# Kernel tuning notes

Measured on AMD Instinct MI355X. Metric: run time of the kernel, lower is better.

## Reference

```python
import jax, jax.numpy as jnp
import numpy as np

NUM_AUDIOS = 64
NODES_PER = 800
N = NUM_AUDIOS * NODES_PER  # 51200
DEG = 8
E = N * DEG  # 409600
IN_C, HID, OUT, HEADS = 512, 256, 256, 2
NEG_SLOPE = 0.2  # PyG GATConv default


def setup_inputs() -> dict:
    key = jax.random.key(0)
    ks = jax.random.split(key, 12)
    x = jax.random.normal(ks[0], (N, IN_C), jnp.float32)
    # edges strictly inside each audio's node block (PyG batching: no cross-graph edges)
    src_l = jax.random.randint(ks[1], (NUM_AUDIOS, NODES_PER * DEG), 0, NODES_PER)
    dst_l = jax.random.randint(ks[2], (NUM_AUDIOS, NODES_PER * DEG), 0, NODES_PER)
    off = (jnp.arange(NUM_AUDIOS) * NODES_PER)[:, None]
    edge_index = jnp.stack([(src_l + off).reshape(-1), (dst_l + off).reshape(-1)]).astype(jnp.int32)
    batch = jnp.repeat(jnp.arange(NUM_AUDIOS), NODES_PER).astype(jnp.int32)

    def gl(k, shape, fan):
        return (jax.random.normal(k, shape, jnp.float32) / np.sqrt(fan)).astype(jnp.float32)

    W1 = gl(ks[3], (IN_C, HEADS * HID), IN_C)
    a_s1 = gl(ks[4], (HEADS, HID), HID)
    a_d1 = gl(ks[5], (HEADS, HID), HID)
    b1 = jnp.zeros((HID,), jnp.float32)
    W2 = gl(ks[6], (HID, HEADS * OUT), HID)
    a_s2 = gl(ks[7], (HEADS, OUT), OUT)
    a_d2 = gl(ks[8], (HEADS, OUT), OUT)
    b2 = jnp.zeros((OUT,), jnp.float32)
    w_att = gl(ks[9], (OUT, 1), OUT)
    b_att = jnp.zeros((1,), jnp.float32)
    w_cls = gl(ks[10], (OUT, 2), OUT)
    b_cls = jnp.zeros((2,), jnp.float32)
    return dict(x=x, edge_index=edge_index, batch=batch,
                W1=W1, a_s1=a_s1, a_d1=a_d1, b1=b1,
                W2=W2, a_s2=a_s2, a_d2=a_d2, b2=b2,
                w_att=w_att, b_att=b_att, w_cls=w_cls, b_cls=b_cls)


def _gat(x, src, dst, W, a_s, a_d, b):
    """PyG GATConv(heads=H, concat=False): linear -> per-edge LeakyReLU scores ->
    softmax over incoming edges (with self-loops) -> scatter-sum -> head-mean + bias."""
    n = x.shape[0]
    H, C = a_s.shape
    h = (x @ W).reshape(n, H, C)                      # [N,H,C]
    al_s = jnp.einsum('nhc,hc->nh', h, a_s)           # [N,H]
    al_d = jnp.einsum('nhc,hc->nh', h, a_d)
    loop = jnp.arange(n, dtype=src.dtype)             # add self-loops (default)
    s = jnp.concatenate([src, loop])
    d = jnp.concatenate([dst, loop])
    e = jax.nn.leaky_relu(al_s[s] + al_d[d], NEG_SLOPE)  # [E+N,H]
    mx = jax.ops.segment_max(e, d, num_segments=n)
    w = jnp.exp(e - mx[d])
    den = jax.ops.segment_sum(w, d, num_segments=n)
    alpha = w / den[d]
    out = jax.ops.segment_sum(h[s] * alpha[:, :, None], d, num_segments=n)  # [N,H,C]
    return out.mean(axis=1) + b


def reference(x, edge_index, batch, W1, a_s1, a_d1, b1, W2, a_s2, a_d2, b2,
              w_att, b_att, w_cls, b_cls):
    src, dst = edge_index[0], edge_index[1]
    h = jax.nn.relu(_gat(x, src, dst, W1, a_s1, a_d1, b1))
    node_emb = _gat(h, src, dst, W2, a_s2, a_d2, b2)
    # per-audio temporal attention: softmax over nodes within each audio segment.
    # (edges never cross audio boundaries, so the per-subgraph GAT re-run in the
    #  original Python loop equals the full-graph GAT restricted to each segment.)
    logits = node_emb @ w_att + b_att                 # [N,1]
    mx = jax.ops.segment_max(logits, batch, num_segments=NUM_AUDIOS)
    w = jnp.exp(logits - mx[batch])
    den = jax.ops.segment_sum(w, batch, num_segments=NUM_AUDIOS)
    attn = w / den[batch]                             # [N,1]
    attended = jax.ops.segment_sum(attn * node_emb, batch, num_segments=NUM_AUDIOS)  # [A,OUT]
    audio_result = attended @ w_cls + b_cls           # [A,2]
    return node_emb, audio_result
```

## Files before the change

### kernel.cpp

```cpp
#include <hip/hip_runtime.h>
#include <cstdint>
#include <cstddef>

#define NUM_AUDIOS 64
#define NODES_PER  800
#define NN         51200
#define EE         409600

typedef __attribute__((ext_vector_type(8))) unsigned short ushort8;
typedef __attribute__((ext_vector_type(8))) __bf16 bf16x8;
typedef __attribute__((ext_vector_type(4))) float f32x4;

__device__ __forceinline__ float b2f(unsigned short h) {
  return __uint_as_float(((unsigned)h) << 16);
}
__device__ __forceinline__ unsigned short f2b(float f) {
  unsigned u = __float_as_uint(f);
  u += 0x7fffu + ((u >> 16) & 1u);
  return (unsigned short)(u >> 16);
}
__device__ __forceinline__ float lrelu(float v) { return v > 0.f ? v : 0.2f * v; }

#define P_AS1 0
#define P_AD1 512
#define P_B1  1024
#define P_AS2 1536
#define P_AD2 2048
#define P_B2  2560
#define P_WATT 3072
#define P_BATT 3328
#define P_WCLS 3336
#define P_BCLS 3848

#define ZERO_F4 132096
#define ZERO_BLOCKS 516

__global__ __launch_bounds__(256) void prolog0_k(float4* __restrict__ zbase,
                                                 const unsigned short* __restrict__ x,
                                                 int* __restrict__ flag) {
  const int i = blockIdx.x * 256 + threadIdx.x;
  if (i < ZERO_F4) zbase[i] = (float4){0.f, 0.f, 0.f, 0.f};
  if (blockIdx.x == 0) {
    __shared__ int s;
    if (threadIdx.x == 0) s = 0;
    __syncthreads();
    int big = 0;
    for (int k = threadIdx.x; k < 4096; k += 256) {
      const float v = b2f(x[k]);
      if (!(__builtin_fabsf(v) <= 1e4f)) big = 1;
    }
    if (big) atomicOr(&s, 1);
    __syncthreads();
    if (threadIdx.x == 0) *flag = s;
  }
}

#define PB_PAR  10
#define PB_T1   (PB_PAR + 1024)
#define PB_T2   (PB_T1 + 512)
#define PB_HIST (PB_T2 + 1600)

__global__ __launch_bounds__(256) void prep_k(
    const void* __restrict__ W1, unsigned short* __restrict__ W1T,
    const void* __restrict__ W2, unsigned short* __restrict__ W2T,
    const void* p0, const void* p1, const void* p2, const void* p3, const void* p4,
    const void* p5, const void* p6, const void* p7, const void* p8, const void* p9,
    unsigned short* __restrict__ params,
    const int* __restrict__ dst, int* __restrict__ counts,
    const int* __restrict__ flagp) {
  const int b = blockIdx.x, tid = threadIdx.x;
  const int f = *flagp;
  if (b < PB_PAR) {
    const void* srcs[10] = {p0, p1, p2, p3, p4, p5, p6, p7, p8, p9};
    const int offs[10] = {P_AS1, P_AD1, P_B1, P_AS2, P_AD2, P_B2, P_WATT, P_BATT, P_WCLS, P_BCLS};
    const int lens[10] = {512, 512, 256, 512, 512, 256, 256, 1, 512, 2};
    const int s = b;
    for (int i = tid; i < lens[s]; i += 256)
      params[offs[s] + i] = f ? f2b(((const float*)srcs[s])[i])
                              : ((const unsigned short*)srcs[s])[i];
  } else if (b < PB_T1) {
    const int idx = (b - PB_PAR) * 256 + tid;
    const int n = idx >> 9, k = idx & 511;
    W1T[idx] = f ? f2b(((const float*)W1)[(size_t)k * 512 + n])
                 : ((const unsigned short*)W1)[(size_t)k * 512 + n];
  } else if (b < PB_T2) {
    const int idx = (b - PB_T1) * 256 + tid;
    const int n = idx >> 8, k = idx & 255;
    W2T[idx] = f ? f2b(((const float*)W2)[(size_t)k * 512 + n])
                 : ((const unsigned short*)W2)[(size_t)k * 512 + n];
  } else {
    const int e = (b - PB_T2) * 256 + tid;
    atomicAdd(&counts[dst[e]], 1);
  }
}

__global__ __launch_bounds__(256) void rowptr_k(const int* __restrict__ counts, int* __restrict__ row_ptr) {
  __shared__ int sh[800];
  __shared__ int pre[200];
  const int a = blockIdx.x, t = threadIdx.x;
  for (int i = t; i < 800; i += 256) sh[i] = counts[a * 800 + i];
  __syncthreads();
  if (t < 200) pre[t] = sh[t * 4] + sh[t * 4 + 1] + sh[t * 4 + 2] + sh[t * 4 + 3];
  __syncthreads();
  if (t == 0) {
    int run = 0;
    for (int i = 0; i < 200; ++i) { const int v = pre[i]; pre[i] = run; run += v; }
  }
  __syncthreads();
  if (t < 200) {
    int b = a * 6400 + pre[t];
#pragma unroll
    for (int j = 0; j < 4; ++j) { row_ptr[a * 800 + t * 4 + j] = b; b += sh[t * 4 + j]; }
  }
}

__global__ __launch_bounds__(256) void scatter_k(const int* __restrict__ src, const int* __restrict__ dst,
                                                 const int* __restrict__ row_ptr, int* __restrict__ cursor,
                                                 int* __restrict__ ssrc) {
  const int e = blockIdx.x * 256 + threadIdx.x;
  const int d = dst[e];
  const int p = atomicAdd(&cursor[d], 1);
  ssrc[row_ptr[d] + p] = src[e];
}

__device__ __forceinline__ void mfma_tile256(const unsigned short* As, const unsigned short* Bs,
                                             int wm, int wn, int row, int quad, f32x4 acc[8][4]) {
  bf16x8 af[8], bq[4];
  const int pa = (quad ^ (row & 3)) * 8;
#pragma unroll
  for (int i = 0; i < 8; ++i)
    af[i] = *(const bf16x8*)&As[(wm * 128 + i * 16 + row) * 32 + pa];
#pragma unroll
  for (int j = 0; j < 4; ++j)
    bq[j] = *(const bf16x8*)&Bs[(wn * 64 + j * 16 + row) * 32 + pa];
#pragma unroll
  for (int i = 0; i < 8; ++i)
#pragma unroll
    for (int j = 0; j < 4; ++j)
      acc[i][j] = __builtin_amdgcn_mfma_f32_16x16x32_bf16(af[i], bq[j], acc[i][j], 0, 0, 0);
}

__global__ __launch_bounds__(512, 2) void gemm_bt(const void* __restrict__ Araw,
                                                  const unsigned short* __restrict__ BT,
                                                  unsigned short* __restrict__ C,
                                                  int K, int Nn,
                                                  const unsigned short* __restrict__ a_s,
                                                  const unsigned short* __restrict__ a_d,
                                                  float* __restrict__ al_s,
                                                  float* __restrict__ al_d,
                                                  const int* __restrict__ aflag) {
  __shared__ unsigned short smem[32768];
  const int tid = threadIdx.x;
  const int wave = tid >> 6, lane = tid & 63;
  const int bid = blockIdx.x;
  const int g = bid & 7, bt = bid >> 3;
  const int mt = bt >> 1, nt = bt & 1;
  const int m0 = (g * 25 + mt) * 256;
  const int n0 = nt * 256;
  const int wm = wave >> 2, wn = wave & 3;
  const int row = lane & 15, quad = lane >> 4;
  const int col = lane & 15;
  f32x4 acc[8][4];
#pragma unroll
  for (int i = 0; i < 8; ++i)
#pragma unroll
    for (int j = 0; j < 4; ++j) acc[i][j] = (f32x4){0.f, 0.f, 0.f, 0.f};

  const bool a_is_f32 = (aflag != nullptr) && (*aflag != 0);
  const unsigned short* A16 = (const unsigned short*)Araw;
  const float* A32 = (const float*)Araw;
  const int srow0 = tid >> 2;
  const int kph = tid & 3;

  if (!a_is_f32) {
    const int nk = K >> 5;
    auto stage = [&](int buf, int k0) {
      unsigned short* Asb = smem + buf * 16384;
      unsigned short* Bsb = Asb + 8192;
#pragma unroll
      for (int p = 0; p < 2; ++p) {
        const int arow = p * 128 + srow0;
        const int kc = ((kph ^ (arow & 3)) * 8);
        __builtin_amdgcn_global_load_lds(
            (const __attribute__((address_space(1))) void*)(A16 + (size_t)(m0 + arow) * K + k0 + kc),
            (__attribute__((address_space(3))) void*)(Asb + (p * 512 + tid) * 8),
            16, 0, 0);
        __builtin_amdgcn_global_load_lds(
            (const __attribute__((address_space(1))) void*)(BT + (size_t)(n0 + arow) * K + k0 + kc),
            (__attribute__((address_space(3))) void*)(Bsb + (p * 512 + tid) * 8),
            16, 0, 0);
      }
    };
    stage(0, 0);
    for (int t = 0; t < nk; ++t) {
      const int cur = t & 1;
      if (t + 1 < nk) {
        stage(cur ^ 1, (t + 1) << 5);
        asm volatile("s_waitcnt vmcnt(4)" ::: "memory");
      } else {
        asm volatile("s_waitcnt vmcnt(0)" ::: "memory");
      }
      __builtin_amdgcn_sched_barrier(0);
      __builtin_amdgcn_s_barrier();
      __builtin_amdgcn_sched_barrier(0);
      mfma_tile256(smem + cur * 16384, smem + cur * 16384 + 8192, wm, wn, row, quad, acc);
      __builtin_amdgcn_sched_barrier(0);
      __builtin_amdgcn_s_barrier();
    }
  } else {
    unsigned short* As = smem;
    unsigned short* Bs = smem + 8192;
    for (int k0 = 0; k0 < K; k0 += 32) {
      ushort8 pk[2];
#pragma unroll
      for (int p = 0; p < 2; ++p) {
        const int arow = p * 128 + srow0;
        const int kc = ((kph ^ (arow & 3)) * 8);
        const float* ap = A32 + (size_t)(m0 + arow) * K + k0 + kc;
        const float4 f0 = *(const float4*)ap;
        const float4 f1 = *(const float4*)(ap + 4);
        pk[p][0] = f2b(f0.x); pk[p][1] = f2b(f0.y); pk[p][2] = f2b(f0.z); pk[p][3] = f2b(f0.w);
        pk[p][4] = f2b(f1.x); pk[p][5] = f2b(f1.y); pk[p][6] = f2b(f1.z); pk[p][7] = f2b(f1.w);
      }
      __syncthreads();
#pragma unroll
      for (int p = 0; p < 2; ++p) {
        const int arow = p * 128 + srow0;
        const int kc = ((kph ^ (arow & 3)) * 8);
        __builtin_amdgcn_global_load_lds(
            (const __attribute__((address_space(1))) void*)(BT + (size_t)(n0 + arow) * K + k0 + kc),
            (__attribute__((address_space(3))) void*)(Bs + (size_t)(p * 512 + tid) * 8),
            16, 0, 0);
        *(ushort8*)&As[(size_t)(p * 512 + tid) * 8] = pk[p];
      }
      __syncthreads();
      mfma_tile256(As, Bs, wm, wn, row, quad, acc);
    }
  }

  __syncthreads();

  {
    float* alb = (float*)smem;
    float as4[4], ad4[4];
#pragma unroll
    for (int j = 0; j < 4; ++j) {
      const int gn = n0 + wn * 64 + j * 16 + col;
      as4[j] = b2f(a_s[gn]);
      ad4[j] = b2f(a_d[gn]);
    }
#pragma unroll
    for (int i = 0; i < 8; ++i)
#pragma unroll
      for (int r = 0; r < 4; ++r) {
        float ps = 0.f, pd = 0.f;
#pragma unroll
        for (int j = 0; j < 4; ++j) { ps += acc[i][j][r] * as4[j]; pd += acc[i][j][r] * ad4[j]; }
#pragma unroll
        for (int off = 1; off < 16; off <<= 1) {
          ps += __shfl_xor(ps, off);
          pd += __shfl_xor(pd, off);
        }
        if (col == 0) {
          const int rr = wm * 128 + i * 16 + quad * 4 + r;
          alb[(0 * 4 + wn) * 256 + rr] = ps;
          alb[(1 * 4 + wn) * 256 + rr] = pd;
        }
      }
  }
  __syncthreads();
  {
    const float* alb = (const float*)smem;
    const int rr = tid >> 1, kind = tid & 1;
    float s = 0.f;
#pragma unroll
    for (int w = 0; w < 4; ++w) s += alb[(kind * 4 + w) * 256 + rr];
    float* dstp = kind ? al_d : al_s;
    dstp[(size_t)(m0 + rr) * 2 + nt] = s;
  }
  __syncthreads();

#pragma unroll
  for (int half = 0; half < 2; ++half) {
    if (wm == half) {
#pragma unroll
      for (int i = 0; i < 8; ++i)
#pragma unroll
        for (int jj = 0; jj < 4; ++jj)
#pragma unroll
          for (int r = 0; r < 4; ++r) {
            const int rl = i * 16 + quad * 4 + r;
            const int pc = (wn * 4 + jj) ^ quad;
            smem[rl * 256 + pc * 16 + col] = f2b(acc[i][jj][r]);
          }
    }
    __syncthreads();
#pragma unroll
    for (int s = 0; s < 8; ++s) {
      const int u = tid + 512 * s;
      const int rw = u >> 5, unit = u & 31;
      const int lc = unit >> 1, h16 = unit & 1;
      const int q = (rw >> 2) & 3;
      const ushort8 v = *(const ushort8*)&smem[rw * 256 + ((lc ^ q) * 16 + h16 * 8)];
      *(ushort8*)&C[(size_t)(m0 + half * 128 + rw) * Nn + n0 + unit * 8] = v;
    }
    __syncthreads();
  }
}

__global__ __launch_bounds__(256) void agg_k(const unsigned short* __restrict__ h,
                                             const float* __restrict__ al_s, const float* __restrict__ al_d,
                                             const int* __restrict__ row_ptr, const int* __restrict__ counts,
                                             const int* __restrict__ ssrc, const unsigned short* __restrict__ bias,
                                             unsigned short* __restrict__ out, int do_relu,
                                             void* __restrict__ out2, const int* __restrict__ flagp,
                                             const unsigned short* __restrict__ watt,
                                             float* __restrict__ lg) {
  const int wave = threadIdx.x >> 6, lane = threadIdx.x & 63;
  const int b = blockIdx.x;
  const int g = b & 7, r = b >> 3;
  const int a = g + 8 * (r / 200);
  const int chunk = r % 200;
  const int n = a * 800 + chunk * 4 + wave;
  const int head = lane >> 5;
  const int hl = lane & 31;
  const int hsel = lane & 32;
  const int deg = counts[n];
  const int base = row_ptr[n];
  const float ald = al_d[n * 2 + head];
  const float self_e = lrelu(al_s[n * 2 + head] + ald);

  float m = -1e30f;
  for (int i = hl; i < deg; i += 32) {
    const int s = ssrc[base + i];
    m = fmaxf(m, al_s[s * 2 + head]);
  }
#pragma unroll
  for (int off = 1; off < 32; off <<= 1) m = fmaxf(m, __shfl_xor(m, off));
  const float mx = fmaxf(lrelu(m + ald), self_e);

  const float w_self = __expf(self_e - mx);
  float acc[8];
  {
    const ushort8 hv = *(const ushort8*)&h[(unsigned)(n * 512 + lane * 8)];
#pragma unroll
    for (int j = 0; j < 8; ++j) acc[j] = w_self * b2f(hv[j]);
  }
  float dpart = 0.f;
  for (int t0 = 0; t0 < deg; t0 += 32) {
    const int cnt = min(32, deg - t0);
    int s = 0; float w = 0.f;
    if (hl < cnt) {
      s = ssrc[base + t0 + hl];
      w = __expf(lrelu(al_s[s * 2 + head] + ald) - mx);
      dpart += w;
    }
    for (int i = 0; i < cnt; ++i) {
      const float wb = __shfl(w, hsel + i);
      const int sb = __shfl(s, hsel + i);
      const ushort8 hv = *(const ushort8*)&h[(unsigned)(sb * 512 + lane * 8)];
#pragma unroll
      for (int j = 0; j < 8; ++j) acc[j] += wb * b2f(hv[j]);
    }
  }
#pragma unroll
  for (int off = 1; off < 32; off <<= 1) dpart += __shfl_xor(dpart, off);
  const float inv = 1.f / (w_self + dpart);

  const int c0 = hl * 8;
  ushort8 res;
  float ov[8];
#pragma unroll
  for (int j = 0; j < 8; ++j) {
    const float mine = acc[j] * inv;
    const float other = __shfl_xor(mine, 32);
    float o = (mine + other) * 0.5f + b2f(bias[c0 + j]);
    if (do_relu) o = fmaxf(o, 0.f);
    ov[j] = o;
    res[j] = f2b(o);
  }
  if (lane < 32) {
    *(ushort8*)&out[(unsigned)(n * 256 + c0)] = res;
    if (out2) {
      if (*flagp) {
        float4* p = (float4*)((float*)out2 + (size_t)n * 256 + c0);
        p[0] = (float4){ov[0], ov[1], ov[2], ov[3]};
        p[1] = (float4){ov[4], ov[5], ov[6], ov[7]};
      } else {
        *(ushort8*)((unsigned short*)out2 + (size_t)n * 256 + c0) = res;
      }
    }
    if (lg) {
      const ushort8 wv = *(const ushort8*)&watt[c0];
      float d = 0.f;
#pragma unroll
      for (int j = 0; j < 8; ++j) d += ov[j] * b2f(wv[j]);
#pragma unroll
      for (int off = 1; off < 32; off <<= 1) d += __shfl_xor(d, off);
      if (hl == 0) lg[n] = d + b2f(watt[256]);
    }
  }
}

__global__ __launch_bounds__(256) void stats_k(const float* __restrict__ lg,
                                               float* __restrict__ mxv, float* __restrict__ invv) {
  __shared__ float red[256];
  const int a = blockIdx.x, t = threadIdx.x;
  float m = -1e30f;
  for (int i = t; i < 800; i += 256) m = fmaxf(m, lg[a * 800 + i]);
  red[t] = m; __syncthreads();
  for (int s = 128; s >= 1; s >>= 1) { if (t < s) red[t] = fmaxf(red[t], red[t + s]); __syncthreads(); }
  const float mx = red[0];
  __syncthreads();
  float sum = 0.f;
  for (int i = t; i < 800; i += 256) sum += __expf(lg[a * 800 + i] - mx);
  red[t] = sum; __syncthreads();
  for (int s = 128; s >= 1; s >>= 1) { if (t < s) red[t] += red[t + s]; __syncthreads(); }
  if (t == 0) { mxv[a] = mx; invv[a] = 1.f / red[0]; }
}

__global__ __launch_bounds__(256) void attended_k(const unsigned short* __restrict__ emb,
                                                  const float* __restrict__ lg,
                                                  const float* __restrict__ mxv,
                                                  const float* __restrict__ invv,
                                                  float* __restrict__ attended) {
  const int b = blockIdx.x;
  const int a = b >> 3, chunk = b & 7;
  const int t = threadIdx.x;
  __shared__ float ws[100];
  const int i0 = chunk * 100;
  const float mx = mxv[a], inv = invv[a];
  if (t < 100) ws[t] = __expf(lg[a * 800 + i0 + t] - mx) * inv;
  __syncthreads();
  float acc = 0.f;
  const unsigned short* base = emb + ((size_t)(a * 800 + i0)) * 256 + t;
#pragma unroll 4
  for (int j = 0; j < 100; ++j) acc += ws[j] * b2f(base[(size_t)j * 256]);
  atomicAdd(&attended[a * 256 + t], acc);
}

__global__ __launch_bounds__(256) void cls_k(const float* __restrict__ attended,
                                             const unsigned short* __restrict__ params,
                                             void* __restrict__ out, const int* __restrict__ flag) {
  __shared__ float red[256];
  const int a = blockIdx.x, t = threadIdx.x;
  const float v = attended[a * 256 + t];
  const float p0 = v * b2f(params[P_WCLS + t * 2]);
  const float p1 = v * b2f(params[P_WCLS + t * 2 + 1]);
  red[t] = p0; __syncthreads();
  for (int s = 128; s >= 1; s >>= 1) { if (t < s) red[t] += red[t + s]; __syncthreads(); }
  const float r0 = red[0];
  __syncthreads();
  red[t] = p1; __syncthreads();
  for (int s = 128; s >= 1; s >>= 1) { if (t < s) red[t] += red[t + s]; __syncthreads(); }
  const float r1 = red[0];
  if (t == 0) {
    const float o0 = r0 + b2f(params[P_BCLS]);
    const float o1 = r1 + b2f(params[P_BCLS + 1]);
    if (*flag) {
      ((float*)out)[(size_t)NN * 256 + a * 2]     = o0;
      ((float*)out)[(size_t)NN * 256 + a * 2 + 1] = o1;
    } else {
      ((unsigned short*)out)[(size_t)NN * 256 + a * 2]     = f2b(o0);
      ((unsigned short*)out)[(size_t)NN * 256 + a * 2 + 1] = f2b(o1);
    }
  }
}

extern "C" void kernel_launch(void* const* d_in, const int* in_sizes, int n_in,
                              void* d_out, int out_size, void* d_ws, size_t ws_size,
                              hipStream_t stream) {
  (void)in_sizes; (void)n_in; (void)out_size; (void)ws_size;
  const void* x_raw  = d_in[0];
  const int*  eidx   = (const int*)d_in[1];
  const int* src = eidx;
  const int* dst = eidx + EE;

  char* ws = (char*)d_ws;
  size_t off = 0;
  auto alloc = [&](size_t bytes) -> void* {
    void* p = ws + off;
    off += (bytes + 255) & ~(size_t)255;
    return p;
  };
  int* flag              = (int*)alloc(256);
  unsigned short* params = (unsigned short*)alloc(4096 * 2);
  unsigned short* W1T    = (unsigned short*)alloc((size_t)512 * 512 * 2);
  unsigned short* W2T    = (unsigned short*)alloc((size_t)512 * 256 * 2);
  unsigned short* scr    = (unsigned short*)alloc((size_t)NN * 512 * 2);
  unsigned short* hbig   = (unsigned short*)alloc((size_t)NN * 512 * 2);
  int*   counts   = (int*)alloc((size_t)NN * 4);
  int*   cursor   = (int*)alloc((size_t)NN * 4);
  float* attended = (float*)alloc((size_t)NUM_AUDIOS * 256 * 4);
  float* al_s1    = (float*)alloc((size_t)NN * 2 * 4);
  float* al_d1    = (float*)alloc((size_t)NN * 2 * 4);
  float* al_s2    = (float*)alloc((size_t)NN * 2 * 4);
  float* al_d2    = (float*)alloc((size_t)NN * 2 * 4);
  int*   rowp   = (int*)alloc((size_t)NN * 4);
  int*   ssrc   = (int*)alloc((size_t)EE * 4);
  float* lg     = (float*)alloc((size_t)NN * 4);
  float* mxv    = (float*)alloc(NUM_AUDIOS * 4);
  float* invv   = (float*)alloc(NUM_AUDIOS * 4);
  unsigned short* hrel  = scr;
  unsigned short* emb16 = scr + (size_t)NN * 256;

  prolog0_k<<<dim3(ZERO_BLOCKS), 256, 0, stream>>>((float4*)counts,
                                                   (const unsigned short*)x_raw, flag);

  prep_k<<<dim3(PB_HIST), 256, 0, stream>>>(
      d_in[3], W1T, d_in[7], W2T,
      d_in[4], d_in[5], d_in[6], d_in[8], d_in[9],
      d_in[10], d_in[11], d_in[12], d_in[13], d_in[14],
      params, dst, counts, flag);

  rowptr_k<<<dim3(NUM_AUDIOS), 256, 0, stream>>>(counts, rowp);
  scatter_k<<<dim3(EE / 256), 256, 0, stream>>>(src, dst, rowp, cursor, ssrc);

  gemm_bt<<<dim3(400), 512, 0, stream>>>(x_raw, W1T, hbig, 512, 512,
                                         params + P_AS1, params + P_AD1, al_s1, al_d1, flag);
  agg_k<<<dim3(NN / 4), 256, 0, stream>>>(hbig, al_s1, al_d1, rowp, counts, ssrc,
                                          params + P_B1, hrel, 1, nullptr, flag,
                                          params + P_WATT, nullptr);

  gemm_bt<<<dim3(400), 512, 0, stream>>>(hrel, W2T, hbig, 256, 512,
                                         params + P_AS2, params + P_AD2, al_s2, al_d2, nullptr);
  agg_k<<<dim3(NN / 4), 256, 0, stream>>>(hbig, al_s2, al_d2, rowp, counts, ssrc,
                                          params + P_B2, emb16, 0, d_out, flag,
                                          params + P_WATT, lg);

  stats_k<<<dim3(NUM_AUDIOS), 256, 0, stream>>>(lg, mxv, invv);
  attended_k<<<dim3(NUM_AUDIOS * 8), 256, 0, stream>>>(emb16, lg, mxv, invv, attended);
  cls_k<<<dim3(NUM_AUDIOS), 256, 0, stream>>>(attended, params, d_out, flag);
}
```

Baseline: 426.6 us.

## Deepen GEMM K-step to 64 with an 8-way swizzled LDS layout and setprio

The bf16 GEMM path now stages 64-wide K slices per pipeline step instead of 32, doubling LDS to 128KB with a new XOR-8 swizzle. Each step issues twice the async global-to-LDS loads and two MFMA sub-passes, which halves the number of barrier and wait rounds. It also raises wave priority around the MFMA block. The larger LDS footprint may cut occupancy below the two blocks per CU declared in launch_bounds.

```diff
diff --git a/kernel.cpp b/kernel.cpp
--- a/kernel.cpp
+++ b/kernel.cpp
@@ -140,6 +140,31 @@
       acc[i][j] = __builtin_amdgcn_mfma_f32_16x16x32_bf16(af[i], bq[j], acc[i][j], 0, 0, 0);
 }
 
+__device__ __forceinline__ void mfma_k64(const unsigned short* Ab, const unsigned short* Bb,
+                                         int wm, int wn, int row, int quad, f32x4 acc[8][4]) {
+#pragma unroll
+  for (int kh = 0; kh < 2; ++kh) {
+    bf16x8 af[8], bq[4];
+#pragma unroll
+    for (int i = 0; i < 8; ++i) {
+      const int R = wm * 128 + i * 16 + row;
+      const int p = (kh * 4 + quad) ^ (R & 7);
+      af[i] = *(const bf16x8*)&Ab[(R * 8 + p) * 8];
+    }
+#pragma unroll
+    for (int j = 0; j < 4; ++j) {
+      const int R = wn * 64 + j * 16 + row;
+      const int p = (kh * 4 + quad) ^ (R & 7);
+      bq[j] = *(const bf16x8*)&Bb[(R * 8 + p) * 8];
+    }
+#pragma unroll
+    for (int i = 0; i < 8; ++i)
+#pragma unroll
+      for (int j = 0; j < 4; ++j)
+        acc[i][j] = __builtin_amdgcn_mfma_f32_16x16x32_bf16(af[i], bq[j], acc[i][j], 0, 0, 0);
+  }
+}
+
 __global__ __launch_bounds__(512, 2) void gemm_bt(const void* __restrict__ Araw,
                                                   const unsigned short* __restrict__ BT,
                                                   unsigned short* __restrict__ C,
@@ -149,7 +174,7 @@
                                                   float* __restrict__ al_s,
                                                   float* __restrict__ al_d,
                                                   const int* __restrict__ aflag) {
-  __shared__ unsigned short smem[32768];
+  __shared__ unsigned short smem[65536];
   const int tid = threadIdx.x;
   const int wave = tid >> 6, lane = tid & 63;
   const int bid = blockIdx.x;
@@ -169,47 +194,50 @@
   const bool a_is_f32 = (aflag != nullptr) && (*aflag != 0);
   const unsigned short* A16 = (const unsigned short*)Araw;
   const float* A32 = (const float*)Araw;
-  const int srow0 = tid >> 2;
-  const int kph = tid & 3;
 
   if (!a_is_f32) {
-    const int nk = K >> 5;
-    auto stage = [&](int buf, int k0) {
-      unsigned short* Asb = smem + buf * 16384;
-      unsigned short* Bsb = Asb + 8192;
-#pragma unroll
-      for (int p = 0; p < 2; ++p) {
-        const int arow = p * 128 + srow0;
-        const int kc = ((kph ^ (arow & 3)) * 8);
+    const int nk = K >> 6;
+    auto stage64 = [&](int buf, int k0) {
+      unsigned short* Ab = smem + buf * 32768;
+      unsigned short* Bb = Ab + 16384;
+#pragma unroll
+      for (int ld = 0; ld < 4; ++ld) {
+        const int cc = ld * 512 + tid;
+        const int rw = cc >> 3, ch = cc & 7;
+        const int kc = ((ch ^ (rw & 7)) * 8);
         __builtin_amdgcn_global_load_lds(
-            (const __attribute__((address_space(1))) void*)(A16 + (size_t)(m0 + arow) * K + k0 + kc),
-            (__attribute__((address_space(3))) void*)(Asb + (p * 512 + tid) * 8),
+            (const __attribute__((address_space(1))) void*)(A16 + (size_t)(m0 + rw) * K + k0 + kc),
+            (__attribute__((address_space(3))) void*)(Ab + (size_t)cc * 8),
             16, 0, 0);
         __builtin_amdgcn_global_load_lds(
-            (const __attribute__((address_space(1))) void*)(BT + (size_t)(n0 + arow) * K + k0 + kc),
-            (__attribute__((address_space(3))) void*)(Bsb + (p * 512 + tid) * 8),
+            (const __attribute__((address_space(1))) void*)(BT + (size_t)(n0 + rw) * K + k0 + kc),
+            (__attribute__((address_space(3))) void*)(Bb + (size_t)cc * 8),
             16, 0, 0);
       }
     };
-    stage(0, 0);
+    stage64(0, 0);
     for (int t = 0; t < nk; ++t) {
-      const int cur = t & 1;
       if (t + 1 < nk) {
-        stage(cur ^ 1, (t + 1) << 5);
-        asm volatile("s_waitcnt vmcnt(4)" ::: "memory");
+        stage64((t + 1) & 1, (t + 1) << 6);
+        asm volatile("s_waitcnt vmcnt(8)" ::: "memory");
       } else {
         asm volatile("s_waitcnt vmcnt(0)" ::: "memory");
       }
       __builtin_amdgcn_sched_barrier(0);
       __builtin_amdgcn_s_barrier();
       __builtin_amdgcn_sched_barrier(0);
-      mfma_tile256(smem + cur * 16384, smem + cur * 16384 + 8192, wm, wn, row, quad, acc);
+      __builtin_amdgcn_s_setprio(1);
+      mfma_k64(smem + (t & 1) * 32768, smem + (t & 1) * 32768 + 16384,
+               wm, wn, row, quad, acc);
+      __builtin_amdgcn_s_setprio(0);
       __builtin_amdgcn_sched_barrier(0);
       __builtin_amdgcn_s_barrier();
     }
   } else {
     unsigned short* As = smem;
     unsigned short* Bs = smem + 8192;
+    const int srow0 = tid >> 2;
+    const int kph = tid & 3;
     for (int k0 = 0; k0 < K; k0 += 32) {
       ushort8 pk[2];
 #pragma unroll
```

New measurement: 422.8 us. About the same (-0.9%).
